# Kernel tuning notes

Hardware: AMD Instinct MI355X
Metric: run time of the kernel (lower is better)

Reference implementation:

```python
import jax, jax.numpy as jnp
import numpy as np

N_HEADS = 16


def setup_inputs() -> dict:
    key = jax.random.key(0)
    k1, k2, k3 = jax.random.split(key, 3)
    B, N, D = 2, 2048, 1024
    x = jax.random.normal(k1, (B, N, D), dtype=jnp.float32)
    w_qkv = jax.random.normal(k2, (D, 3 * D), dtype=jnp.float32) * (D ** -0.5)
    w_proj = jax.random.normal(k3, (D, D), dtype=jnp.float32) * (D ** -0.5)
    return {"x": x, "w_qkv": w_qkv, "w_proj": w_proj}


def _rotate_half(t):
    # interleaved-pair rotation: (x1, x2) -> (-x2, x1)
    shp = t.shape
    t2 = t.reshape(*shp[:-1], shp[-1] // 2, 2)
    return jnp.stack((-t2[..., 1], t2[..., 0]), axis=-1).reshape(shp)


def reference(x, w_qkv, w_proj):
    B, N, D = x.shape
    H = N_HEADS
    hd = D // H
    qkv = x @ w_qkv                                   # [B, N, 3D]
    qkv = qkv.reshape(B, N, 3, H, hd).transpose(2, 0, 3, 1, 4)
    q, k, v = qkv[0], qkv[1], qkv[2]                  # [B, H, N, hd]

    inv_freq = 1.0 / (10000.0 ** (jnp.arange(0, hd, 2, dtype=jnp.float32) / hd))
    freqs = jnp.arange(N, dtype=jnp.float32)[:, None] * inv_freq[None, :]  # [N, hd/2]
    sin = jnp.repeat(jnp.sin(freqs), 2, axis=-1)[None, None]               # [1,1,N,hd]
    cos = jnp.repeat(jnp.cos(freqs), 2, axis=-1)[None, None]

    q = q * cos + _rotate_half(q) * sin
    k = k * cos + _rotate_half(k) * sin

    scale = hd ** -0.5
    attn = jax.nn.softmax(jnp.einsum('bhqd,bhkd->bhqk', q, k) * scale, axis=-1)
    out = jnp.einsum('bhqk,bhkd->bhqd', attn, v)      # [B, H, N, hd]
    out = out.transpose(0, 2, 1, 3).reshape(B, N, D)
    return out @ w_proj
```

## Files before the change

kernel.cpp:

```cpp
#include <hip/hip_runtime.h>
#include <hip/hip_bf16.h>
#include <cstdint>
#include <cmath>

#define DEVINL __device__ __forceinline__

typedef __attribute__((ext_vector_type(8)))  __bf16 b8;
typedef __attribute__((ext_vector_type(4)))  float  f4;
typedef __attribute__((ext_vector_type(16))) float  f16v;
typedef __attribute__((ext_vector_type(4)))  unsigned int u32x4;

DEVINL unsigned short f2bf(float f){
  unsigned int u = __float_as_uint(f);
  u += 0x7FFFu + ((u >> 16) & 1u);
  return (unsigned short)(u >> 16);
}

DEVINL void gl_lds16(const void* g, void* l){
  __builtin_amdgcn_global_load_lds(
      (const __attribute__((address_space(1))) void*)g,
      (__attribute__((address_space(3))) void*)l, 16, 0, 0);
}

DEVINL f4 mfma16(b8 a, b8 b, f4 c){
  return __builtin_amdgcn_mfma_f32_16x16x32_bf16(a, b, c, 0, 0, 0);
}
DEVINL f16v mfma32(b8 a, b8 b, f16v c){
  return __builtin_amdgcn_mfma_f32_32x32x16_bf16(a, b, c, 0, 0, 0);
}

DEVINL float exp2a(float x){
  float r; asm("v_exp_f32 %0, %1" : "=v"(r) : "v"(x)); return r;
}
DEVINL unsigned int cvtpk(float lo, float hi){
  unsigned int r; asm("v_cvt_pk_bf16_f32 %0, %1, %2" : "=v"(r) : "v"(lo), "v"(hi)); return r;
}
DEVINL void plswap(unsigned int &a, unsigned int &b){
  asm("v_permlane32_swap_b32 %0, %1" : "+v"(a), "+v"(b));
}

#define BARRAW() asm volatile("s_barrier" ::: "memory")
#define WCNT(N)  asm volatile("s_waitcnt vmcnt(" #N ")" ::: "memory")


__global__ __launch_bounds__(256) void prep_k(const float* __restrict__ x,
                                              const float* __restrict__ wqkv,
                                              const float* __restrict__ wproj,
                                              unsigned short* __restrict__ xb,
                                              unsigned short* __restrict__ wqkvT,
                                              unsigned short* __restrict__ wprojT,
                                              float2* __restrict__ rtab){
  __shared__ float t[32][33];
  const int b = blockIdx.x, tid = threadIdx.x;
  if (b < 1024){
    int i = b * 256 + tid;
    #pragma unroll
    for (int it = 0; it < 4; it++){
      float4 v = ((const float4*)x)[i];
      ushort4 o; o.x = f2bf(v.x); o.y = f2bf(v.y); o.z = f2bf(v.z); o.w = f2bf(v.w);
      ((ushort4*)xb)[i] = o;
      i += 1024 * 256;
    }
  } else if (b < 5120){
    const float* in; unsigned short* out; int N2, tt;
    if (b < 4096){ in = wqkv;  out = wqkvT;  N2 = 3072; tt = b - 1024; }
    else         { in = wproj; out = wprojT; N2 = 1024; tt = b - 4096; }
    const int K2 = 1024;
    int nx = (tt % (N2 / 32)) * 32, kx = (tt / (N2 / 32)) * 32;
    int tx = tid & 31, ty = tid >> 5;
    #pragma unroll
    for (int i2 = 0; i2 < 4; i2++)
      t[ty + 8 * i2][tx] = in[(size_t)(kx + ty + 8 * i2) * N2 + nx + tx];
    __syncthreads();
    #pragma unroll
    for (int i2 = 0; i2 < 4; i2++)
      out[(size_t)(nx + ty + 8 * i2) * K2 + kx + tx] = f2bf(t[tx][ty + 8 * i2]);
  } else {
    int tr = (b - 5120) * 256 + tid;
    int n = tr >> 5, i2 = tr & 31;
    float invf = expf(-(float)i2 * (9.210340371976184f / 32.0f));
    float ph = (float)n * invf;
    float s, c;
    sincosf(ph, &s, &c);
    rtab[tr] = make_float2(c, s);
  }
}


template<int NREP, int EPI>
__global__ __launch_bounds__(512, 2) void gemm256_k(const unsigned short* __restrict__ A,
                                                    const unsigned short* __restrict__ Bt, int N,
                                                    float* __restrict__ Of,
                                                    unsigned short* __restrict__ Qg,
                                                    unsigned short* __restrict__ Kg,
                                                    unsigned short* __restrict__ Vt,
                                                    const float2* __restrict__ rtab){
  constexpr int K = 1024;
  __shared__ unsigned short As[2][256 * 64];
  __shared__ unsigned short Bs[2][NREP * 64 * 64];
  const int tid = threadIdx.x, w = tid >> 6, l = tid & 63;
  const int wm = w >> 2, wn = w & 3;
  const int id = blockIdx.x + blockIdx.y * 16;
  const int xcd = id & 7, jj2 = id >> 3;
  const int mblk = (xcd >> 1) * 4 + (jj2 >> 3);
  const int nblk = (xcd & 1) * 8 + (jj2 & 7);
  const int m0 = mblk * 256, n0 = nblk * (NREP * 64);

  f4 acc[8][NREP];
  const f4 fz = {0.f, 0.f, 0.f, 0.f};
  #pragma unroll
  for (int i = 0; i < 8; i++)
    #pragma unroll
    for (int j = 0; j < NREP; j++) acc[i][j] = fz;

  const int srow8 = (l >> 3);
  const int ssrc  = ((l & 7) ^ (srow8 & 7)) * 8;

  auto stage = [&](int slot, int kt){
    const unsigned short* Ab = A + kt * 64 + ssrc;
    #pragma unroll
    for (int c2 = 0; c2 < 4; c2++){
      int ch = w * 4 + c2;
      gl_lds16(Ab + (size_t)(m0 + ch * 8 + srow8) * K, (char*)&As[slot][0] + ch * 1024);
    }
    const unsigned short* Bb = Bt + kt * 64 + ssrc;
    #pragma unroll
    for (int c2 = 0; c2 < NREP; c2++){
      int ch = w * NREP + c2;
      gl_lds16(Bb + (size_t)(n0 + ch * 8 + srow8) * K, (char*)&Bs[slot][0] + ch * 1024);
    }
  };

  auto compute = [&](int slot){
    const char* At  = (const char*)&As[slot][0];
    const char* Btl = (const char*)&Bs[slot][0];
    #pragma unroll
    for (int kk = 0; kk < 2; kk++){
      b8 af[8], bf[NREP];
      int sb = kk * 4 + (l >> 4);
      #pragma unroll
      for (int mi = 0; mi < 8; mi++){
        int r = wm * 128 + mi * 16 + (l & 15);
        af[mi] = *(const b8*)(At + r * 128 + ((sb ^ (r & 7)) * 16));
      }
      #pragma unroll
      for (int ni = 0; ni < NREP; ni++){
        int r = wn * (NREP * 16) + ni * 16 + (l & 15);
        bf[ni] = *(const b8*)(Btl + r * 128 + ((sb ^ (r & 7)) * 16));
      }
      __builtin_amdgcn_s_setprio(1);
      #pragma unroll
      for (int mi = 0; mi < 8; mi++)
        #pragma unroll
        for (int ni = 0; ni < NREP; ni++)
          acc[mi][ni] = mfma16(af[mi], bf[ni], acc[mi][ni]);
      __builtin_amdgcn_s_setprio(0);
    }
  };

  auto wcnt_stg = [&](){
    if constexpr (NREP == 4)      WCNT(8);
    else if constexpr (NREP == 3) WCNT(7);
    else if constexpr (NREP == 2) WCNT(6);
    else                          WCNT(5);
  };

  stage(0, 0);
  stage(1, 1);
  wcnt_stg();
  BARRAW();
  for (int i = 0; i < 8; i++){
    compute(0);
    BARRAW();
    if (i < 7){ stage(0, 2 * i + 2); wcnt_stg(); }
    else      { WCNT(0); }
    BARRAW();
    compute(1);
    BARRAW();
    if (i < 7){ stage(1, 2 * i + 3); wcnt_stg(); }
    BARRAW();
  }

  if constexpr (EPI == 0){
    const float qscale = 0.18033688011112042f;
    const int bb2 = m0 >> 11;
    #pragma unroll
    for (int mi = 0; mi < 8; mi++){
      #pragma unroll
      for (int ni = 0; ni < NREP; ni++){
        f4 a = acc[mi][ni];
        int c = n0 + wn * (NREP * 16) + ni * 16 + (l & 15);
        int s = c >> 10;
        int d = c & 63, h = (c >> 6) & 15;
        if (s == 2){
          int ns0 = (m0 & 2047) + wm * 128 + mi * 16 + (l >> 4) * 4;
          ushort4 pv;
          pv.x = f2bf(a[0]); pv.y = f2bf(a[1]); pv.z = f2bf(a[2]); pv.w = f2bf(a[3]);
          *(ushort4*)(Vt + (((size_t)(bb2 * 16 + h) * 64 + d) << 11) + ns0) = pv;
        } else {
          #pragma unroll
          for (int jj = 0; jj < 4; jj++){
            int m = m0 + wm * 128 + mi * 16 + (l >> 4) * 4 + jj;
            int bb = m >> 11, ns = m & 2047;
            size_t didx = ((size_t)(bb * 16 + h) * 2048 + ns) * 64 + d;
            float part = __shfl_xor(a[jj], 1);
            float2 cs = rtab[ns * 32 + (d >> 1)];
            float val = (d & 1) ? (a[jj] * cs.x + part * cs.y)
                                : (a[jj] * cs.x - part * cs.y);
            if (s == 0){ Qg[didx] = f2bf(val * qscale); }
            else       { Kg[didx] = f2bf(val); }
          }
        }
      }
    }
  } else {
    #pragma unroll
    for (int mi = 0; mi < 8; mi++)
      #pragma unroll
      for (int ni = 0; ni < NREP; ni++){
        int c = n0 + wn * (NREP * 16) + ni * 16 + (l & 15);
        #pragma unroll
        for (int jj = 0; jj < 4; jj++){
          int m = m0 + wm * 128 + mi * 16 + (l >> 4) * 4 + jj;
          Of[(size_t)m * N + c] = acc[mi][ni][jj];
        }
      }
  }
}


__global__ __launch_bounds__(256) void attn_k(const unsigned short* __restrict__ Qg,
                                              const unsigned short* __restrict__ Kg,
                                              const unsigned short* __restrict__ Vt,
                                              unsigned short* __restrict__ Ao){
  __shared__ unsigned short Ks[3][4096];
  __shared__ unsigned short Vs[3][4096];
  const int tid = threadIdx.x, w = tid >> 6, l = tid & 63;
  const int l31 = l & 31, lam = l >> 5;

  const int id = blockIdx.x + blockIdx.y * 16;
  const int xc = id & 7, j = id >> 3;
  const int g = xc * 4 + (j & 3), qb = j >> 2;
  const int q0 = qb * 128 + w * 32;
  const size_t hb = (size_t)g << 17;

  b8 qf[4];
  {
    const unsigned short* qrow = Qg + hb + (size_t)(q0 + l31) * 64 + lam * 8;
    #pragma unroll
    for (int kd = 0; kd < 4; kd++) qf[kd] = *(const b8*)(qrow + kd * 16);
  }

  const unsigned short* kgb = Kg + hb;
  const unsigned short* vgb = Vt + hb;
  const int srow = (l >> 3);
  const int sc8  = ((l & 7) ^ (srow & 7)) * 8;

  auto stage = [&](int buf, int kv0){
    #pragma unroll
    for (int c = 0; c < 2; c++){
      int chunk = w * 2 + c;
      int r = chunk * 8 + srow;
      gl_lds16(kgb + (size_t)(kv0 + r) * 64 + sc8,
               (char*)&Ks[buf][0] + chunk * 1024);
      gl_lds16(vgb + (size_t)r * 2048 + kv0 + sc8,
               (char*)&Vs[buf][0] + chunk * 1024);
    }
  };

  union { u32x4 u; b8 v; } ones;
  ones.u[0] = ones.u[1] = ones.u[2] = ones.u[3] = 0x3F803F80u;

  f16v O[2], L;
  #pragma unroll
  for (int i = 0; i < 16; i++){ O[0][i] = 0.f; O[1][i] = 0.f; L[i] = 0.f; }

  auto tile = [&](int buf){
    b8 kf[8], vf[8];
    const char* ksb = (const char*)&Ks[buf][0];
    const char* vsb = (const char*)&Vs[buf][0];
    const int rsw = (l31 & 7);
    #pragma unroll
    for (int kvb = 0; kvb < 2; kvb++)
      #pragma unroll
      for (int kd = 0; kd < 4; kd++)
        kf[kvb * 4 + kd] = *(const b8*)(ksb + (kvb * 32 + l31) * 128
                                        + (((kd * 2 + lam) ^ rsw) * 16));
    #pragma unroll
    for (int s = 0; s < 4; s++)
      #pragma unroll
      for (int db = 0; db < 2; db++)
        vf[s * 2 + db] = *(const b8*)(vsb + (db * 32 + l31) * 128
                                      + (((2 * s + lam) ^ rsw) * 16));

    f16v st[2];
    #pragma unroll
    for (int i = 0; i < 16; i++){ st[0][i] = 0.f; st[1][i] = 0.f; }
    #pragma unroll
    for (int kd = 0; kd < 4; kd++) st[0] = mfma32(kf[kd],     qf[kd], st[0]);
    #pragma unroll
    for (int kd = 0; kd < 4; kd++) st[1] = mfma32(kf[4 + kd], qf[kd], st[1]);

    #pragma unroll
    for (int b2 = 0; b2 < 2; b2++)
      #pragma unroll
      for (int r = 0; r < 16; r++)
        st[b2][r] = exp2a(st[b2][r]);

    #pragma unroll
    for (int s = 0; s < 4; s++){
      const int b = s >> 1, base = (s & 1) * 8;
      unsigned int pA = cvtpk(st[b][base + 0], st[b][base + 1]);
      unsigned int pB = cvtpk(st[b][base + 2], st[b][base + 3]);
      unsigned int pC = cvtpk(st[b][base + 4], st[b][base + 5]);
      unsigned int pD = cvtpk(st[b][base + 6], st[b][base + 7]);
      plswap(pA, pC); plswap(pB, pD);
      union { u32x4 u; b8 v; } pf;
      pf.u[0] = pA; pf.u[1] = pB; pf.u[2] = pC; pf.u[3] = pD;
      O[0] = mfma32(pf.v, vf[s * 2 + 0], O[0]);
      O[1] = mfma32(pf.v, vf[s * 2 + 1], O[1]);
      L    = mfma32(pf.v, ones.v,       L);
    }
  };

  stage(0, 0); stage(1, 64);
  WCNT(4); BARRAW();
  #pragma unroll 1
  for (int t = 0; t < 30; t += 3){
    stage(2, (t + 2) * 64); tile(0); WCNT(4); BARRAW();
    stage(0, (t + 3) * 64); tile(1); WCNT(4); BARRAW();
    stage(1, (t + 4) * 64); tile(2); WCNT(4); BARRAW();
  }
  tile(0);
  WCNT(0); BARRAW();
  tile(1);

  const int bb = g >> 4, h = g & 15;
  unsigned short* aoBase = Ao + (size_t)bb * 2048 * 1024 + h * 64 + l31;
  #pragma unroll
  for (int r = 0; r < 16; r++){
    int qr = (r & 3) + 8 * (r >> 2) + 4 * lam;
    float li = 1.0f / L[r];
    size_t rowoff = (size_t)(q0 + qr) * 1024;
    aoBase[rowoff]      = f2bf(O[0][r] * li);
    aoBase[rowoff + 32] = f2bf(O[1][r] * li);
  }
}


extern "C" void kernel_launch(void* const* d_in, const int* in_sizes, int n_in,
                              void* d_out, int out_size, void* d_ws, size_t ws_size,
                              hipStream_t stream){
  const float* x     = (const float*)d_in[0];
  const float* wqkv  = (const float*)d_in[1];
  const float* wproj = (const float*)d_in[2];
  float* out = (float*)d_out;

  if (ws_size < 42467328u) return;
  char* ws = (char*)d_ws;
  unsigned short* xb     = (unsigned short*)(ws);
  unsigned short* wqkvT  = (unsigned short*)(ws + 8388608);
  unsigned short* wprojT = (unsigned short*)(ws + 14680064);
  float2*         rtab   = (float2*)(ws + 16777216);
  unsigned short* Qg     = (unsigned short*)(ws + 17301504);
  unsigned short* Kg     = (unsigned short*)(ws + 25690112);
  unsigned short* Vt     = (unsigned short*)(ws + 34078720);
  unsigned short* Ao     = xb;

  prep_k<<<5376, 256, 0, stream>>>(x, wqkv, wproj, xb, wqkvT, wprojT, rtab);
  gemm256_k<3, 0><<<dim3(16, 16), 512, 0, stream>>>(xb, wqkvT, 3072, nullptr, Qg, Kg, Vt, rtab);
  attn_k<<<dim3(16, 32), 256, 0, stream>>>(Qg, Kg, Vt, Ao);
  gemm256_k<1, 1><<<dim3(16, 16), 512, 0, stream>>>(Ao, wprojT, 1024, out, nullptr, nullptr, nullptr, nullptr);
}
```

Measured before the change: 111.3 us.

## Reshape GEMM wave tiling to 4x2 and double-buffer attention K/V staging

The GEMM kernel's wave layout changes from 2x4 (each wave 128 rows by NREP*16 columns) to 4x2 (64 rows by NREP*32 columns). This changes the ratio of A to B fragment loads from LDS per MFMA. The attention kernel drops from a triple-buffered K/V ring, where the next stage is issued while computing, to double buffering with barriers around each stage. That cuts LDS use, which may allow more resident blocks, but it serializes loads and compute more and adds barriers.

```diff
diff --git a/kernel.cpp b/kernel.cpp
--- a/kernel.cpp
+++ b/kernel.cpp
@@ -96,22 +96,23 @@
                                                     unsigned short* __restrict__ Vt,
                                                     const float2* __restrict__ rtab){
   constexpr int K = 1024;
+  constexpr int NR2 = 2 * NREP;
   __shared__ unsigned short As[2][256 * 64];
   __shared__ unsigned short Bs[2][NREP * 64 * 64];
   const int tid = threadIdx.x, w = tid >> 6, l = tid & 63;
-  const int wm = w >> 2, wn = w & 3;
+  const int wm = w >> 1, wn = w & 1;
   const int id = blockIdx.x + blockIdx.y * 16;
   const int xcd = id & 7, jj2 = id >> 3;
   const int mblk = (xcd >> 1) * 4 + (jj2 >> 3);
   const int nblk = (xcd & 1) * 8 + (jj2 & 7);
   const int m0 = mblk * 256, n0 = nblk * (NREP * 64);
 
-  f4 acc[8][NREP];
+  f4 acc[4][NR2];
   const f4 fz = {0.f, 0.f, 0.f, 0.f};
   #pragma unroll
-  for (int i = 0; i < 8; i++)
-    #pragma unroll
-    for (int j = 0; j < NREP; j++) acc[i][j] = fz;
+  for (int i = 0; i < 4; i++)
+    #pragma unroll
+    for (int j = 0; j < NR2; j++) acc[i][j] = fz;
 
   const int srow8 = (l >> 3);
   const int ssrc  = ((l & 7) ^ (srow8 & 7)) * 8;
@@ -136,23 +137,23 @@
     const char* Btl = (const char*)&Bs[slot][0];
     #pragma unroll
     for (int kk = 0; kk < 2; kk++){
-      b8 af[8], bf[NREP];
+      b8 af[4], bf[NR2];
       int sb = kk * 4 + (l >> 4);
       #pragma unroll
-      for (int mi = 0; mi < 8; mi++){
-        int r = wm * 128 + mi * 16 + (l & 15);
+      for (int mi = 0; mi < 4; mi++){
+        int r = wm * 64 + mi * 16 + (l & 15);
         af[mi] = *(const b8*)(At + r * 128 + ((sb ^ (r & 7)) * 16));
       }
       #pragma unroll
-      for (int ni = 0; ni < NREP; ni++){
-        int r = wn * (NREP * 16) + ni * 16 + (l & 15);
+      for (int ni = 0; ni < NR2; ni++){
+        int r = wn * (NREP * 32) + ni * 16 + (l & 15);
         bf[ni] = *(const b8*)(Btl + r * 128 + ((sb ^ (r & 7)) * 16));
       }
       __builtin_amdgcn_s_setprio(1);
       #pragma unroll
-      for (int mi = 0; mi < 8; mi++)
+      for (int mi = 0; mi < 4; mi++)
         #pragma unroll
-        for (int ni = 0; ni < NREP; ni++)
+        for (int ni = 0; ni < NR2; ni++)
           acc[mi][ni] = mfma16(af[mi], bf[ni], acc[mi][ni]);
       __builtin_amdgcn_s_setprio(0);
     }
@@ -185,22 +186,22 @@
     const float qscale = 0.18033688011112042f;
     const int bb2 = m0 >> 11;
     #pragma unroll
-    for (int mi = 0; mi < 8; mi++){
-      #pragma unroll
-      for (int ni = 0; ni < NREP; ni++){
+    for (int mi = 0; mi < 4; mi++){
+      #pragma unroll
+      for (int ni = 0; ni < NR2; ni++){
         f4 a = acc[mi][ni];
-        int c = n0 + wn * (NREP * 16) + ni * 16 + (l & 15);
+        int c = n0 + wn * (NREP * 32) + ni * 16 + (l & 15);
         int s = c >> 10;
         int d = c & 63, h = (c >> 6) & 15;
         if (s == 2){
-          int ns0 = (m0 & 2047) + wm * 128 + mi * 16 + (l >> 4) * 4;
+          int ns0 = (m0 & 2047) + wm * 64 + mi * 16 + (l >> 4) * 4;
           ushort4 pv;
           pv.x = f2bf(a[0]); pv.y = f2bf(a[1]); pv.z = f2bf(a[2]); pv.w = f2bf(a[3]);
           *(ushort4*)(Vt + (((size_t)(bb2 * 16 + h) * 64 + d) << 11) + ns0) = pv;
         } else {
           #pragma unroll
           for (int jj = 0; jj < 4; jj++){
-            int m = m0 + wm * 128 + mi * 16 + (l >> 4) * 4 + jj;
+            int m = m0 + wm * 64 + mi * 16 + (l >> 4) * 4 + jj;
             int bb = m >> 11, ns = m & 2047;
             size_t didx = ((size_t)(bb * 16 + h) * 2048 + ns) * 64 + d;
             float part = __shfl_xor(a[jj], 1);
@@ -215,13 +216,13 @@
     }
   } else {
     #pragma unroll
-    for (int mi = 0; mi < 8; mi++)
-      #pragma unroll
-      for (int ni = 0; ni < NREP; ni++){
-        int c = n0 + wn * (NREP * 16) + ni * 16 + (l & 15);
+    for (int mi = 0; mi < 4; mi++)
+      #pragma unroll
+      for (int ni = 0; ni < NR2; ni++){
+        int c = n0 + wn * (NREP * 32) + ni * 16 + (l & 15);
         #pragma unroll
         for (int jj = 0; jj < 4; jj++){
-          int m = m0 + wm * 128 + mi * 16 + (l >> 4) * 4 + jj;
+          int m = m0 + wm * 64 + mi * 16 + (l >> 4) * 4 + jj;
           Of[(size_t)m * N + c] = acc[mi][ni][jj];
         }
       }
@@ -233,8 +234,8 @@
                                               const unsigned short* __restrict__ Kg,
                                               const unsigned short* __restrict__ Vt,
                                               unsigned short* __restrict__ Ao){
-  __shared__ unsigned short Ks[3][4096];
-  __shared__ unsigned short Vs[3][4096];
+  __shared__ unsigned short Ks[2][4096];
+  __shared__ unsigned short Vs[2][4096];
   const int tid = threadIdx.x, w = tid >> 6, l = tid & 63;
   const int l31 = l & 31, lam = l >> 5;
 
@@ -323,17 +324,21 @@
     }
   };
 
-  stage(0, 0); stage(1, 64);
-  WCNT(4); BARRAW();
-  #pragma unroll 1
-  for (int t = 0; t < 30; t += 3){
-    stage(2, (t + 2) * 64); tile(0); WCNT(4); BARRAW();
-    stage(0, (t + 3) * 64); tile(1); WCNT(4); BARRAW();
-    stage(1, (t + 4) * 64); tile(2); WCNT(4); BARRAW();
-  }
-  tile(0);
-  WCNT(0); BARRAW();
-  tile(1);
+  stage(0, 0);
+  stage(1, 64);
+  WCNT(4);
+  BARRAW();
+  for (int i = 0; i < 16; i++){
+    tile(0);
+    BARRAW();
+    if (i < 15){ stage(0, (2 * i + 2) * 64); WCNT(4); }
+    else       { WCNT(0); }
+    BARRAW();
+    tile(1);
+    BARRAW();
+    if (i < 15){ stage(1, (2 * i + 3) * 64); WCNT(4); }
+    BARRAW();
+  }
 
   const int bb = g >> 4, h = g & 15;
   unsigned short* aoBase = Ao + (size_t)bb * 2048 * 1024 + h * 64 + l31;
```

New measurement: 106.4 us, median of 3. -4.4%, faster.
